# Performance work log

Measured on AMD Instinct MI355X. Metric: run time of the kernel, lower is better.

Reference implementation:

```python
import jax, jax.numpy as jnp
import numpy as np

N, E, H, C = 100000, 800000, 128, 128


def setup_inputs() -> dict:
    key = jax.random.key(0)
    ks = jax.random.split(key, 8)
    x = jax.random.normal(ks[0], (N, H), dtype=jnp.float32)
    edge_index = jax.random.randint(ks[1], (2, E), 0, N, dtype=jnp.int32)
    s = 0.02
    w_lead = jax.random.normal(ks[2], (H,), dtype=jnp.float32) * s
    b_lead = jnp.zeros((), dtype=jnp.float32)
    w1 = jax.random.normal(ks[3], (H, H), dtype=jnp.float32) * s
    b1 = jnp.zeros((H,), dtype=jnp.float32)
    w2 = jax.random.normal(ks[4], (H, C), dtype=jnp.float32) * s
    b2 = jnp.zeros((C,), dtype=jnp.float32)
    return {"x": x, "edge_index": edge_index, "w_lead": w_lead, "b_lead": b_lead,
            "w1": w1, "b1": b1, "w2": w2, "b2": b2}


def reference(x, edge_index, w_lead, b_lead, w1, b1, w2, b2):
    num_nodes = x.shape[0]
    row, col = edge_index[0], edge_index[1]
    ar = jnp.arange(num_nodes, dtype=row.dtype)

    # leader election logits per node
    logits = x @ w_lead + b_lead  # [N]

    # extended edge list with self loops (guarantees every squad non-empty)
    src_ext = jnp.concatenate([row, ar])
    dst_ext = jnp.concatenate([col, ar])

    # scatter_max over incoming edges: per-dst max logit, argmax = winning src node
    e_logit = logits[src_ext]
    seg_max = jax.ops.segment_max(e_logit, dst_ext, num_segments=num_nodes)
    cand = jnp.where(e_logit == seg_max[dst_ext], src_ext, -1)
    leader_idx = jax.ops.segment_max(cand, dst_ext, num_segments=num_nodes)
    leader_idx = jnp.where(leader_idx < 0, ar, leader_idx)  # empty-squad fallback: self

    # scatter_mean neighbor aggregation (original edges only)
    sums = jax.ops.segment_sum(x[row], col, num_segments=num_nodes)  # [N,H]
    cnt = jax.ops.segment_sum(jnp.ones_like(col, dtype=x.dtype), col, num_segments=num_nodes)
    neigh_mean = sums / jnp.maximum(cnt, 1.0)[:, None]

    # squad report MLP (computed densely; only leader rows are ever gathered,
    # identical math to the masked-subset version in the original)
    h = jax.nn.gelu(neigh_mean @ w1 + b1, approximate=False)
    reports = h @ w2 + b2  # [N,C]

    # each agent reads its squad leader's report
    return reports[leader_idx]
```

## Files before the change

kernel.cpp:

```cpp
#include <hip/hip_runtime.h>
#include <math.h>

#define H128 128
#define NBLK 64
#define BKT 256
#define MAXNB 512

typedef short bf16x8 __attribute__((ext_vector_type(8)));
typedef unsigned short u16x8 __attribute__((ext_vector_type(8)));
typedef float f32x4 __attribute__((ext_vector_type(4)));

__device__ __forceinline__ unsigned long long enc64(double d) {
    unsigned long long b = (unsigned long long)__double_as_longlong(d);
    return (b & 0x8000000000000000ULL) ? ~b : (b | 0x8000000000000000ULL);
}

__device__ __forceinline__ unsigned short f2bf(float f) {
    unsigned u = __float_as_uint(f);
    return (unsigned short)((u + 0x7FFFu + ((u >> 16) & 1u)) >> 16);
}

__device__ __forceinline__ float bf2f(unsigned short b) {
    return __uint_as_float((unsigned)b << 16);
}

__global__ __launch_bounds__(256) void k_front(const float* __restrict__ x,
        const float* __restrict__ wl, const float* __restrict__ bl,
        unsigned short* __restrict__ xb, double* __restrict__ logits,
        const int* __restrict__ dsts, int* __restrict__ histg,
        int N, int E, int NB, int PB) {
    __shared__ int h[MAXNB];
    if ((int)blockIdx.x < PB) {
        int wave = (int)(blockIdx.x * 4 + (threadIdx.x >> 6));
        int lane = threadIdx.x & 63;
        if (wave >= N) return;
        const float2 v = *reinterpret_cast<const float2*>(x + (size_t)wave * H128 + lane * 2);
        const float2 w = *reinterpret_cast<const float2*>(wl + lane * 2);
        unsigned p = (unsigned)f2bf(v.x) | ((unsigned)f2bf(v.y) << 16);
        *reinterpret_cast<unsigned*>(xb + (size_t)wave * H128 + lane * 2) = p;
        double s = (double)v.x * (double)w.x + (double)v.y * (double)w.y;
#pragma unroll
        for (int off = 32; off > 0; off >>= 1) s += __shfl_down(s, off);
        if (lane == 0) logits[wave] = s + (double)bl[0];
    } else {
        int bid = blockIdx.x - PB;
        for (int i = threadIdx.x; i < NB; i += 256) h[i] = 0;
        __syncthreads();
        int per = (E + NBLK - 1) / NBLK;
        int s = bid * per;
        int e = min(E, s + per);
        for (int j = s + threadIdx.x; j < e; j += 256)
            atomicAdd(&h[dsts[j] >> 8], 1);
        __syncthreads();
        for (int i = threadIdx.x; i < NB; i += 256)
            histg[i * NBLK + bid] = h[i];
    }
}

__global__ __launch_bounds__(MAXNB) void k_offsets(const int* __restrict__ histg,
        int* __restrict__ bstart, int* __restrict__ base, int NB) {
    __shared__ int sm[MAXNB];
    int t = threadIdx.x;
    int tot = 0;
    if (t < NB) {
        const int4* p = reinterpret_cast<const int4*>(histg + t * NBLK);
#pragma unroll
        for (int i = 0; i < NBLK / 4; ++i) { int4 v = p[i]; tot += v.x + v.y + v.z + v.w; }
    }
    sm[t] = tot;
    __syncthreads();
    for (int o = 1; o < MAXNB; o <<= 1) {
        int add = (t >= o) ? sm[t - o] : 0;
        __syncthreads();
        sm[t] += add;
        __syncthreads();
    }
    if (t == 0) bstart[0] = 0;
    if (t < NB) {
        bstart[t + 1] = sm[t];
        int acc = sm[t] - tot;
        const int4* hp = reinterpret_cast<const int4*>(histg + t * NBLK);
        int4* bp = reinterpret_cast<int4*>(base + t * NBLK);
#pragma unroll
        for (int i = 0; i < NBLK / 4; ++i) {
            int4 hv = hp[i];
            int4 o;
            o.x = acc; acc += hv.x;
            o.y = acc; acc += hv.y;
            o.z = acc; acc += hv.z;
            o.w = acc; acc += hv.w;
            bp[i] = o;
        }
    }
}

__global__ __launch_bounds__(256) void k_binscatter(const int* __restrict__ srcs,
        const int* __restrict__ dsts, const int* __restrict__ base,
        unsigned* __restrict__ binned, int E, int NB) {
    __shared__ int cur[MAXNB];
    for (int i = threadIdx.x; i < NB; i += 256)
        cur[i] = base[i * NBLK + blockIdx.x];
    __syncthreads();
    int per = (E + NBLK - 1) / NBLK;
    int s = blockIdx.x * per;
    int e = min(E, s + per);
    for (int j = s + threadIdx.x; j < e; j += 256) {
        int d = dsts[j], r = srcs[j];
        int pos = atomicAdd(&cur[d >> 8], 1);
        binned[pos] = ((unsigned)(d & (BKT - 1)) << 24) | (unsigned)r;
    }
}

__global__ __launch_bounds__(BKT) void k_localize(const unsigned* __restrict__ binned,
        const int* __restrict__ bstart, int* __restrict__ starts,
        int* __restrict__ csr, int N, int E, int NB) {
    __shared__ int deg[BKT];
    __shared__ int sm[BKT];
    __shared__ int cur[BKT];
    int b = blockIdx.x, t = threadIdx.x;
    int s0 = bstart[b], s1 = bstart[b + 1];
    deg[t] = 0;
    __syncthreads();
    for (int j = s0 + t; j < s1; j += BKT)
        atomicAdd(&deg[binned[j] >> 24], 1);
    __syncthreads();
    int v = deg[t];
    sm[t] = v;
    __syncthreads();
    for (int o = 1; o < BKT; o <<= 1) {
        int add = (t >= o) ? sm[t - o] : 0;
        __syncthreads();
        sm[t] += add;
        __syncthreads();
    }
    int excl = sm[t] - v;
    cur[t] = excl;
    int d = b * BKT + t;
    if (d < N) starts[d] = s0 + excl;
    if (b == NB - 1 && t == 0) starts[N] = E;
    __syncthreads();
    for (int j = s0 + t; j < s1; j += BKT) {
        unsigned p = binned[j];
        int pos = atomicAdd(&cur[p >> 24], 1);
        csr[s0 + pos] = (int)(p & 0xFFFFFFu);
    }
}

__global__ __launch_bounds__(256) void k_aggregate(const int* __restrict__ starts,
        const int* __restrict__ csr, const unsigned short* __restrict__ xb,
        const double* __restrict__ logits, unsigned short* __restrict__ meanb,
        int* __restrict__ leader, int N) {
    int d = blockIdx.x * 16 + (threadIdx.x >> 4);
    int lane = threadIdx.x & 15;
    if (d >= N) return;
    int s = starts[d], e = starts[d + 1];
    const unsigned short* xp = xb + lane * 8;
    float a[8];
#pragma unroll
    for (int i = 0; i < 8; ++i) a[i] = 0.f;

    unsigned long long best; int bsrc;
    if (lane == 0) { best = enc64(logits[d]); bsrc = d; }
    else { best = 0ULL; bsrc = -1; }

    int j = s;
    for (; j + 8 <= e; j += 8) {
        int r[8];
#pragma unroll
        for (int q = 0; q < 8; ++q) r[q] = csr[j + q];
        u16x8 v[8];
#pragma unroll
        for (int q = 0; q < 8; ++q)
            v[q] = *reinterpret_cast<const u16x8*>(xp + (size_t)r[q] * H128);
#pragma unroll
        for (int i = 0; i < 8; ++i)
            a[i] += ((bf2f(v[0][i]) + bf2f(v[1][i])) + (bf2f(v[2][i]) + bf2f(v[3][i])))
                  + ((bf2f(v[4][i]) + bf2f(v[5][i])) + (bf2f(v[6][i]) + bf2f(v[7][i])));
        if (lane < 8) {
            int rr = r[lane];
            unsigned long long lg = enc64(logits[rr]);
            if (lg > best || (lg == best && rr > bsrc)) { best = lg; bsrc = rr; }
        }
    }
    for (; j + 2 <= e; j += 2) {
        int r0 = csr[j], r1 = csr[j + 1];
        u16x8 v0 = *reinterpret_cast<const u16x8*>(xp + (size_t)r0 * H128);
        u16x8 v1 = *reinterpret_cast<const u16x8*>(xp + (size_t)r1 * H128);
#pragma unroll
        for (int i = 0; i < 8; ++i) a[i] += bf2f(v0[i]) + bf2f(v1[i]);
        if (lane == 0) {
            unsigned long long lg = enc64(logits[r0]);
            if (lg > best || (lg == best && r0 > bsrc)) { best = lg; bsrc = r0; }
        } else if (lane == 1) {
            unsigned long long lg = enc64(logits[r1]);
            if (lg > best || (lg == best && r1 > bsrc)) { best = lg; bsrc = r1; }
        }
    }
    if (j < e) {
        int r0 = csr[j];
        u16x8 v0 = *reinterpret_cast<const u16x8*>(xp + (size_t)r0 * H128);
#pragma unroll
        for (int i = 0; i < 8; ++i) a[i] += bf2f(v0[i]);
        if (lane == 0) {
            unsigned long long lg = enc64(logits[r0]);
            if (lg > best || (lg == best && r0 > bsrc)) { best = lg; bsrc = r0; }
        }
    }
#pragma unroll
    for (int o = 8; o > 0; o >>= 1) {
        unsigned long long ob = __shfl_xor(best, o);
        int os = __shfl_xor(bsrc, o);
        if (ob > best || (ob == best && os > bsrc)) { best = ob; bsrc = os; }
    }
    if (lane == 0) leader[d] = bsrc;
    float inv = 1.0f / fmaxf((float)(e - s), 1.0f);
    u16x8 mo;
#pragma unroll
    for (int i = 0; i < 8; ++i) mo[i] = f2bf(a[i] * inv);
    *reinterpret_cast<u16x8*>(meanb + (size_t)d * H128 + lane * 8) = mo;
}

__global__ __launch_bounds__(256, 2) void k_gemm_mfma(
        const unsigned short* __restrict__ A, const float* __restrict__ W,
        const float* __restrict__ bias, const int* __restrict__ leader,
        float* __restrict__ outf, unsigned short* __restrict__ outb,
        int N, int dogelu) {
    __shared__ unsigned short wlT[128][136];
    for (int i = threadIdx.x; i < 4096; i += 256) {
        int k = i >> 5;
        int n4 = (i & 31) * 4;
        float4 w = reinterpret_cast<const float4*>(W)[i];
        wlT[n4 + 0][k] = f2bf(w.x);
        wlT[n4 + 1][k] = f2bf(w.y);
        wlT[n4 + 2][k] = f2bf(w.z);
        wlT[n4 + 3][k] = f2bf(w.w);
    }
    __syncthreads();

    const int wid = threadIdx.x >> 6;
    const int lane = threadIdx.x & 63;
    const int row0 = blockIdx.x * 128 + wid * 32;
    const int kblk = (lane >> 4) * 8;

    int rows[2];
#pragma unroll
    for (int t = 0; t < 2; ++t) {
        int node = row0 + t * 16 + (lane & 15);
        int r = (node < N) ? node : (N - 1);
        if (leader) r = leader[r];
        rows[t] = r;
    }

    bf16x8 xf[2][4];
#pragma unroll
    for (int t = 0; t < 2; ++t)
#pragma unroll
        for (int s = 0; s < 4; ++s)
            xf[t][s] = *reinterpret_cast<const bf16x8*>(A + (size_t)rows[t] * H128 + s * 32 + kblk);

    f32x4 acc[2][8];
#pragma unroll
    for (int t = 0; t < 2; ++t)
#pragma unroll
        for (int cb = 0; cb < 8; ++cb)
#pragma unroll
            for (int j = 0; j < 4; ++j) acc[t][cb][j] = 0.0f;

#pragma unroll
    for (int cb = 0; cb < 8; ++cb) {
        const int ch = cb * 16 + (lane & 15);
#pragma unroll
        for (int s = 0; s < 4; ++s) {
            bf16x8 wf = *reinterpret_cast<bf16x8*>(&wlT[ch][s * 32 + kblk]);
            acc[0][cb] = __builtin_amdgcn_mfma_f32_16x16x32_bf16(wf, xf[0][s], acc[0][cb], 0, 0, 0);
            acc[1][cb] = __builtin_amdgcn_mfma_f32_16x16x32_bf16(wf, xf[1][s], acc[1][cb], 0, 0, 0);
        }
    }

    const int chq = (lane >> 4) * 4;
#pragma unroll
    for (int cb = 0; cb < 8; ++cb) {
        const float4 bv = *reinterpret_cast<const float4*>(&bias[cb * 16 + chq]);
#pragma unroll
        for (int t = 0; t < 2; ++t) {
            int node = row0 + t * 16 + (lane & 15);
            if (node >= N) continue;
            float o[4];
            o[0] = acc[t][cb][0] + bv.x;
            o[1] = acc[t][cb][1] + bv.y;
            o[2] = acc[t][cb][2] + bv.z;
            o[3] = acc[t][cb][3] + bv.w;
            if (dogelu) {
#pragma unroll
                for (int j = 0; j < 4; ++j)
                    o[j] = 0.5f * o[j] * (1.0f + erff(o[j] * 0.70710678118654752440f));
            }
            if (outb) {
                ushort4 ov;
                ov.x = f2bf(o[0]); ov.y = f2bf(o[1]); ov.z = f2bf(o[2]); ov.w = f2bf(o[3]);
                *reinterpret_cast<ushort4*>(outb + (size_t)node * H128 + cb * 16 + chq) = ov;
            } else {
                *reinterpret_cast<float4*>(outf + (size_t)node * H128 + cb * 16 + chq) =
                    make_float4(o[0], o[1], o[2], o[3]);
            }
        }
    }
}

extern "C" void kernel_launch(void* const* d_in, const int* in_sizes, int n_in,
                              void* d_out, int out_size, void* d_ws, size_t ws_size,
                              hipStream_t stream) {
    const float* x     = (const float*)d_in[0];
    const int*   ei    = (const int*)d_in[1];
    const float* wlead = (const float*)d_in[2];
    const float* blead = (const float*)d_in[3];
    const float* w1    = (const float*)d_in[4];
    const float* b1    = (const float*)d_in[5];
    const float* w2    = (const float*)d_in[6];
    const float* b2    = (const float*)d_in[7];
    float* out = (float*)d_out;

    const int N = in_sizes[0] / H128;
    const int E = in_sizes[1] / 2;
    const int NB = (N + BKT - 1) / BKT;
    const int PB = (N + 3) / 4;
    const int* srcs = ei;
    const int* dsts = ei + E;

    char* ws = (char*)d_ws;
    size_t off = 0;
    auto alloc = [&](size_t bytes) {
        void* p = ws + off;
        off = (off + bytes + 255) & ~(size_t)255;
        return p;
    };
    unsigned short* xb    = (unsigned short*)alloc((size_t)N * H128 * 2);
    unsigned short* meanb = (unsigned short*)alloc((size_t)N * H128 * 2);
    unsigned short* hbuf  = (unsigned short*)alloc((size_t)N * H128 * 2);
    double* logits = (double*)alloc((size_t)N * 8);
    int* leader = (int*)alloc((size_t)N * 4);
    int* starts = (int*)alloc((size_t)(N + 1) * 4);
    int* csr    = (int*)alloc((size_t)E * 4);
    unsigned* binned = (unsigned*)alloc((size_t)E * 4);
    int* histg  = (int*)alloc((size_t)NB * NBLK * 4);
    int* bstart = (int*)alloc((size_t)(NB + 1) * 4);
    int* base   = (int*)alloc((size_t)NB * NBLK * 4);

    k_front<<<PB + NBLK, 256, 0, stream>>>(x, wlead, blead, xb, logits,
                                           dsts, histg, N, E, NB, PB);

    k_offsets<<<1, MAXNB, 0, stream>>>(histg, bstart, base, NB);
    k_binscatter<<<NBLK, 256, 0, stream>>>(srcs, dsts, base, binned, E, NB);
    k_localize<<<NB, BKT, 0, stream>>>(binned, bstart, starts, csr, N, E, NB);

    k_aggregate<<<(N + 15) / 16, 256, 0, stream>>>(starts, csr, xb, logits, meanb, leader, N);

    k_gemm_mfma<<<(N + 127) / 128, 256, 0, stream>>>(meanb, w1, b1, nullptr, nullptr, hbuf, N, 1);
    k_gemm_mfma<<<(N + 127) / 128, 256, 0, stream>>>(hbuf, w2, b2, leader, out, nullptr, N, 0);
}
```

Measured before the change: 284.7 us.

## Widen histogram/binscatter to more blocks, reorder front blocks, restructure aggregate loop

Raises the number of edge-partition blocks used for the destination histogram and bin scatter, so each block handles fewer edges and more of the GPU is busy. The histogram blocks now come first in k_front's grid so they are scheduled early. In k_aggregate the leader argmax moves out of the 8-wide feature loop into a separate lane-strided pass over the neighbor list, and the feature accumulation is unrolled by 4 instead of 8. This adds a second read of csr and more per-block histogram work in k_offsets, and the shallower unroll leaves fewer gathers in flight.

```diff
diff --git a/kernel.cpp b/kernel.cpp
--- a/kernel.cpp
+++ b/kernel.cpp
@@ -2,7 +2,7 @@
 #include <math.h>
 
 #define H128 128
-#define NBLK 64
+#define NBLK 256
 #define BKT 256
 #define MAXNB 512
 
@@ -28,10 +28,22 @@
         const float* __restrict__ wl, const float* __restrict__ bl,
         unsigned short* __restrict__ xb, double* __restrict__ logits,
         const int* __restrict__ dsts, int* __restrict__ histg,
-        int N, int E, int NB, int PB) {
+        int N, int E, int NB) {
     __shared__ int h[MAXNB];
-    if ((int)blockIdx.x < PB) {
-        int wave = (int)(blockIdx.x * 4 + (threadIdx.x >> 6));
+    if ((int)blockIdx.x < NBLK) {
+        int bid = blockIdx.x;
+        for (int i = threadIdx.x; i < NB; i += 256) h[i] = 0;
+        __syncthreads();
+        int per = (E + NBLK - 1) / NBLK;
+        int s = bid * per;
+        int e = min(E, s + per);
+        for (int j = s + threadIdx.x; j < e; j += 256)
+            atomicAdd(&h[dsts[j] >> 8], 1);
+        __syncthreads();
+        for (int i = threadIdx.x; i < NB; i += 256)
+            histg[i * NBLK + bid] = h[i];
+    } else {
+        int wave = (int)((blockIdx.x - NBLK) * 4 + (threadIdx.x >> 6));
         int lane = threadIdx.x & 63;
         if (wave >= N) return;
         const float2 v = *reinterpret_cast<const float2*>(x + (size_t)wave * H128 + lane * 2);
@@ -42,18 +54,6 @@
 #pragma unroll
         for (int off = 32; off > 0; off >>= 1) s += __shfl_down(s, off);
         if (lane == 0) logits[wave] = s + (double)bl[0];
-    } else {
-        int bid = blockIdx.x - PB;
-        for (int i = threadIdx.x; i < NB; i += 256) h[i] = 0;
-        __syncthreads();
-        int per = (E + NBLK - 1) / NBLK;
-        int s = bid * per;
-        int e = min(E, s + per);
-        for (int j = s + threadIdx.x; j < e; j += 256)
-            atomicAdd(&h[dsts[j] >> 8], 1);
-        __syncthreads();
-        for (int i = threadIdx.x; i < NB; i += 256)
-            histg[i * NBLK + bid] = h[i];
     }
 }
 
@@ -64,7 +64,7 @@
     int tot = 0;
     if (t < NB) {
         const int4* p = reinterpret_cast<const int4*>(histg + t * NBLK);
-#pragma unroll
+#pragma unroll 8
         for (int i = 0; i < NBLK / 4; ++i) { int4 v = p[i]; tot += v.x + v.y + v.z + v.w; }
     }
     sm[t] = tot;
@@ -81,7 +81,7 @@
         int acc = sm[t] - tot;
         const int4* hp = reinterpret_cast<const int4*>(histg + t * NBLK);
         int4* bp = reinterpret_cast<int4*>(base + t * NBLK);
-#pragma unroll
+#pragma unroll 8
         for (int i = 0; i < NBLK / 4; ++i) {
             int4 hv = hp[i];
             int4 o;
@@ -158,53 +158,30 @@
     float a[8];
 #pragma unroll
     for (int i = 0; i < 8; ++i) a[i] = 0.f;
-
+    int j = s;
+    for (; j + 4 <= e; j += 4) {
+        int r0 = csr[j], r1 = csr[j + 1], r2 = csr[j + 2], r3 = csr[j + 3];
+        u16x8 v0 = *reinterpret_cast<const u16x8*>(xp + (size_t)r0 * H128);
+        u16x8 v1 = *reinterpret_cast<const u16x8*>(xp + (size_t)r1 * H128);
+        u16x8 v2 = *reinterpret_cast<const u16x8*>(xp + (size_t)r2 * H128);
+        u16x8 v3 = *reinterpret_cast<const u16x8*>(xp + (size_t)r3 * H128);
+#pragma unroll
+        for (int i = 0; i < 8; ++i)
+            a[i] += (bf2f(v0[i]) + bf2f(v1[i])) + (bf2f(v2[i]) + bf2f(v3[i]));
+    }
+    for (; j < e; ++j) {
+        int r0 = csr[j];
+        u16x8 v0 = *reinterpret_cast<const u16x8*>(xp + (size_t)r0 * H128);
+#pragma unroll
+        for (int i = 0; i < 8; ++i) a[i] += bf2f(v0[i]);
+    }
     unsigned long long best; int bsrc;
     if (lane == 0) { best = enc64(logits[d]); bsrc = d; }
     else { best = 0ULL; bsrc = -1; }
-
-    int j = s;
-    for (; j + 8 <= e; j += 8) {
-        int r[8];
-#pragma unroll
-        for (int q = 0; q < 8; ++q) r[q] = csr[j + q];
-        u16x8 v[8];
-#pragma unroll
-        for (int q = 0; q < 8; ++q)
-            v[q] = *reinterpret_cast<const u16x8*>(xp + (size_t)r[q] * H128);
-#pragma unroll
-        for (int i = 0; i < 8; ++i)
-            a[i] += ((bf2f(v[0][i]) + bf2f(v[1][i])) + (bf2f(v[2][i]) + bf2f(v[3][i])))
-                  + ((bf2f(v[4][i]) + bf2f(v[5][i])) + (bf2f(v[6][i]) + bf2f(v[7][i])));
-        if (lane < 8) {
-            int rr = r[lane];
-            unsigned long long lg = enc64(logits[rr]);
-            if (lg > best || (lg == best && rr > bsrc)) { best = lg; bsrc = rr; }
-        }
-    }
-    for (; j + 2 <= e; j += 2) {
-        int r0 = csr[j], r1 = csr[j + 1];
-        u16x8 v0 = *reinterpret_cast<const u16x8*>(xp + (size_t)r0 * H128);
-        u16x8 v1 = *reinterpret_cast<const u16x8*>(xp + (size_t)r1 * H128);
-#pragma unroll
-        for (int i = 0; i < 8; ++i) a[i] += bf2f(v0[i]) + bf2f(v1[i]);
-        if (lane == 0) {
-            unsigned long long lg = enc64(logits[r0]);
-            if (lg > best || (lg == best && r0 > bsrc)) { best = lg; bsrc = r0; }
-        } else if (lane == 1) {
-            unsigned long long lg = enc64(logits[r1]);
-            if (lg > best || (lg == best && r1 > bsrc)) { best = lg; bsrc = r1; }
-        }
-    }
-    if (j < e) {
-        int r0 = csr[j];
-        u16x8 v0 = *reinterpret_cast<const u16x8*>(xp + (size_t)r0 * H128);
-#pragma unroll
-        for (int i = 0; i < 8; ++i) a[i] += bf2f(v0[i]);
-        if (lane == 0) {
-            unsigned long long lg = enc64(logits[r0]);
-            if (lg > best || (lg == best && r0 > bsrc)) { best = lg; bsrc = r0; }
-        }
+    for (int k2 = s + lane; k2 < e; k2 += 16) {
+        int r = csr[k2];
+        unsigned long long lg = enc64(logits[r]);
+        if (lg > best || (lg == best && r > bsrc)) { best = lg; bsrc = r; }
     }
 #pragma unroll
     for (int o = 8; o > 0; o >>= 1) {
@@ -346,8 +323,8 @@
     int* bstart = (int*)alloc((size_t)(NB + 1) * 4);
     int* base   = (int*)alloc((size_t)NB * NBLK * 4);
 
-    k_front<<<PB + NBLK, 256, 0, stream>>>(x, wlead, blead, xb, logits,
-                                           dsts, histg, N, E, NB, PB);
+    k_front<<<NBLK + PB, 256, 0, stream>>>(x, wlead, blead, xb, logits,
+                                           dsts, histg, N, E, NB);
 
     k_offsets<<<1, MAXNB, 0, stream>>>(histg, bstart, base, NB);
     k_binscatter<<<NBLK, 256, 0, stream>>>(srcs, dsts, base, binned, E, NB);
```

After: 276.2 us. 1.03x faster.
